# Optimization experiments

Measured on AMD Instinct MI355X. Metric: run time of the kernel, lower is better.

## Reference

```python
import jax, jax.numpy as jnp
import numpy as np

N = 16384      # number of PF candidates (nodes)
D_IN = 13      # pfc_input_dim
H = 16         # hidden_dim
K = 8          # kNN neighbors (includes self, dist 0, matching PyG knn(x, x, k))


def setup_inputs() -> dict:
    key = jax.random.key(0)
    ks = jax.random.split(key, 8)

    def w(k, shape):
        return (jax.random.normal(k, shape, dtype=jnp.float32) * 0.1)

    z = lambda n: jnp.zeros((n,), dtype=jnp.float32)
    return {
        "x_pfc": jax.random.normal(ks[0], (N, D_IN), dtype=jnp.float32),
        # pfc_encode: Linear(13,8) SiLU, Linear(8,16) SiLU, Linear(16,15)
        "W1": w(ks[1], (D_IN, H // 2)), "b1": z(H // 2),
        "W2": w(ks[2], (H // 2, H)),    "b2": z(H),
        "W3": w(ks[3], (H, H - 1)),     "b3": z(H - 1),
        # DynamicEdgeConv edge MLP: Linear(2H, H) SiLU
        "We": w(ks[4], (2 * H, H)),     "be": z(H),
        # ffn: Linear(H, 2H) SiLU, Linear(2H, H)
        "Wf1": w(ks[5], (H, 2 * H)),    "bf1": z(2 * H),
        "Wf2": w(ks[6], (2 * H, H)),    "bf2": z(H),
    }


def reference(x_pfc, W1, b1, W2, b2, W3, b3, We, be, Wf1, bf1, Wf2, bf2):
    silu = jax.nn.silu
    # pfc_encode (dropout = identity in eval)
    h = silu(x_pfc @ W1 + b1)
    h = silu(h @ W2 + b2)
    h = h @ W3 + b3                                   # [N, H-1]
    x = jnp.concatenate([h, x_pfc[:, -1:]], axis=1)   # [N, H]

    # Dynamic kNN graph in encoded-feature space (self included, dist 0)
    sq = jnp.sum(x * x, axis=1)                       # [N]
    d2 = sq[:, None] + sq[None, :] - 2.0 * (x @ x.T)  # [N, N] pairwise sq dist
    _, idx = jax.lax.top_k(-d2, K)                    # [N, K] neighbor indices

    # EdgeConv message: nn(cat([x_i, x_j - x_i])), mean aggregation
    x_j = x[idx]                                      # [N, K, H] gather
    x_i = x[:, None, :]                               # [N, 1, H]
    edge_in = jnp.concatenate(
        [jnp.broadcast_to(x_i, x_j.shape), x_j - x_i], axis=-1)  # [N, K, 2H]
    msg = silu(edge_in @ We + be)                     # [N, K, H]
    feats = jnp.mean(msg, axis=1)                     # [N, H]

    # ffn (dropout = identity in eval)
    f = silu(feats @ Wf1 + bf1)
    f = f @ Wf2 + bf2                                 # [N, H]
    return jnp.concatenate([f, x_pfc], axis=1)        # [N, H + D_IN]
```

## Files before the change

### kernel.cpp

```cpp
#include <hip/hip_runtime.h>
#include <math.h>

#define NPTS 16384
#define DIN 13
#define KNN 8
#define GL 12
#define BIGF 1.7014118e38f

typedef _Float16 half8 __attribute__((ext_vector_type(8)));
typedef float f32x4 __attribute__((ext_vector_type(4)));
typedef float f32x16 __attribute__((ext_vector_type(16)));

union HU4 { uint4 u; half8 h; };

__device__ __forceinline__ float silu(float v) {
    return v / (1.0f + __expf(-v));
}

#define MED3(v, a, b) __builtin_amdgcn_fmed3f((v), (a), (b))

#define INS8V(v) {                      \
    d7 = MED3((v), d6, d7);             \
    d6 = MED3((v), d5, d6);             \
    d5 = MED3((v), d4, d5);             \
    d4 = MED3((v), d3, d4);             \
    d3 = MED3((v), d2, d3);             \
    d2 = MED3((v), d1, d2);             \
    d1 = MED3((v), d0, d1);             \
    d0 = fminf((v), d0); }

#define INS12G(v) {                     \
    g11 = MED3((v), g10, g11);          \
    g10 = MED3((v), g9, g10);           \
    g9  = MED3((v), g8, g9);            \
    g8  = MED3((v), g7, g8);            \
    g7  = MED3((v), g6, g7);            \
    g6  = MED3((v), g5, g6);            \
    g5  = MED3((v), g4, g5);            \
    g4  = MED3((v), g3, g4);            \
    g3  = MED3((v), g2, g3);            \
    g2  = MED3((v), g1, g2);            \
    g1  = MED3((v), g0, g1);            \
    g0  = fminf((v), g0); }

#define CSW(p, q) { float lo_ = fminf(m##p, m##q); float hi_ = fmaxf(m##p, m##q); m##p = lo_; m##q = hi_; }

#define CLEAN16() \
    CSW(0,8) CSW(1,9) CSW(2,10) CSW(3,11) CSW(4,12) CSW(5,13) CSW(6,14) CSW(7,15) \
    CSW(0,4) CSW(1,5) CSW(2,6) CSW(3,7) CSW(8,12) CSW(9,13) CSW(10,14) CSW(11,15) \
    CSW(0,2) CSW(1,3) CSW(4,6) CSW(5,7) CSW(8,10) CSW(9,11) CSW(12,14) CSW(13,15) \
    CSW(0,1) CSW(2,3) CSW(4,5) CSW(6,7) CSW(8,9) CSW(10,11) CSW(12,13) CSW(14,15)

#define MERGE12_SHFL(mask) {                                  \
    float b0 = __shfl_xor(g0, (mask), 64);                    \
    float b1 = __shfl_xor(g1, (mask), 64);                    \
    float b2 = __shfl_xor(g2, (mask), 64);                    \
    float b3 = __shfl_xor(g3, (mask), 64);                    \
    float b4 = __shfl_xor(g4, (mask), 64);                    \
    float b5 = __shfl_xor(g5, (mask), 64);                    \
    float b6 = __shfl_xor(g6, (mask), 64);                    \
    float b7 = __shfl_xor(g7, (mask), 64);                    \
    float b8 = __shfl_xor(g8, (mask), 64);                    \
    float b9 = __shfl_xor(g9, (mask), 64);                    \
    float b10 = __shfl_xor(g10, (mask), 64);                  \
    float b11 = __shfl_xor(g11, (mask), 64);                  \
    float m0 = g0, m1 = g1, m2 = g2, m3 = g3;                 \
    float m4 = fminf(g4, b11), m5 = fminf(g5, b10);           \
    float m6 = fminf(g6, b9),  m7 = fminf(g7, b8);            \
    float m8 = fminf(g8, b7),  m9 = fminf(g9, b6);            \
    float m10 = fminf(g10, b5), m11 = fminf(g11, b4);         \
    float m12 = b3, m13 = b2, m14 = b1, m15 = b0;             \
    CLEAN16();                                                \
    g0 = m0; g1 = m1; g2 = m2; g3 = m3; g4 = m4; g5 = m5;     \
    g6 = m6; g7 = m7; g8 = m8; g9 = m9; g10 = m10; g11 = m11; }

#define MERGE12_LDS(LD) {                                     \
    float b0 = LD(0), b1 = LD(1), b2 = LD(2), b3 = LD(3);     \
    float b4 = LD(4), b5 = LD(5), b6 = LD(6), b7 = LD(7);     \
    float b8 = LD(8), b9 = LD(9), b10 = LD(10), b11 = LD(11); \
    float m0 = g0, m1 = g1, m2 = g2, m3 = g3;                 \
    float m4 = fminf(g4, b11), m5 = fminf(g5, b10);           \
    float m6 = fminf(g6, b9),  m7 = fminf(g7, b8);            \
    float m8 = fminf(g8, b7),  m9 = fminf(g9, b6);            \
    float m10 = fminf(g10, b5), m11 = fminf(g11, b4);         \
    float m12 = b3, m13 = b2, m14 = b1, m15 = b0;             \
    CLEAN16();                                                \
    g0 = m0; g1 = m1; g2 = m2; g3 = m3; g4 = m4; g5 = m5;     \
    g6 = m6; g7 = m7; g8 = m8; g9 = m9; g10 = m10; g11 = m11; }

#define MERGE8(mask) {                                   \
    float b0 = __shfl_xor(d0, (mask), 64);               \
    float b1 = __shfl_xor(d1, (mask), 64);               \
    float b2 = __shfl_xor(d2, (mask), 64);               \
    float b3 = __shfl_xor(d3, (mask), 64);               \
    float b4 = __shfl_xor(d4, (mask), 64);               \
    float b5 = __shfl_xor(d5, (mask), 64);               \
    float b6 = __shfl_xor(d6, (mask), 64);               \
    float b7 = __shfl_xor(d7, (mask), 64);               \
    float m0 = fminf(d0, b7), m1 = fminf(d1, b6);        \
    float m2 = fminf(d2, b5), m3 = fminf(d3, b4);        \
    float m4 = fminf(d4, b3), m5 = fminf(d5, b2);        \
    float m6 = fminf(d6, b1), m7 = fminf(d7, b0);        \
    CSW(0,4) CSW(1,5) CSW(2,6) CSW(3,7)                  \
    CSW(0,2) CSW(1,3) CSW(4,6) CSW(5,7)                  \
    CSW(0,1) CSW(2,3) CSW(4,5) CSW(6,7)                  \
    d0 = m0; d1 = m1; d2 = m2; d3 = m3;                  \
    d4 = m4; d5 = m5; d6 = m6; d7 = m7; }

__global__ __launch_bounds__(64) void k_encoder(
    const float* __restrict__ x_pfc,
    const float* __restrict__ W1, const float* __restrict__ b1,
    const float* __restrict__ W2, const float* __restrict__ b2,
    const float* __restrict__ W3, const float* __restrict__ b3,
    const float* __restrict__ We, const float* __restrict__ be,
    float* __restrict__ xo, _Float16* __restrict__ H, _Float16* __restrict__ L,
    _Float16* __restrict__ YH, _Float16* __restrict__ YL,
    float* __restrict__ SQF, unsigned* __restrict__ SQHL,
    float* __restrict__ ACC)
{
    __shared__ float sW1[DIN * 8];
    __shared__ float sb1[8];
    __shared__ float sW2[8 * 16];
    __shared__ float sb2[16];
    __shared__ float sW3[16 * 15];
    __shared__ float sb3[15];
    __shared__ float sWe[16 * 16];
    __shared__ float sbe[16];
    int t = threadIdx.x;
    for (int q = t; q < DIN * 8; q += 64) sW1[q] = W1[q];
    for (int q = t; q < 8; q += 64) sb1[q] = b1[q];
    for (int q = t; q < 8 * 16; q += 64) sW2[q] = W2[q];
    for (int q = t; q < 16; q += 64) sb2[q] = b2[q];
    for (int q = t; q < 16 * 15; q += 64) sW3[q] = W3[q];
    for (int q = t; q < 15; q += 64) sb3[q] = b3[q];
    for (int q = t; q < 16 * 16; q += 64) sWe[q] = We[q];
    for (int q = t; q < 16; q += 64) sbe[q] = be[q];
    __syncthreads();

    int i = blockIdx.x * 64 + t;
    float in[DIN];
#pragma unroll
    for (int d = 0; d < DIN; ++d) in[d] = x_pfc[i * DIN + d];

    float a1[8];
#pragma unroll
    for (int h = 0; h < 8; ++h) a1[h] = sb1[h];
#pragma unroll
    for (int d = 0; d < DIN; ++d) {
        float v = in[d];
#pragma unroll
        for (int h = 0; h < 8; ++h) a1[h] += v * sW1[d * 8 + h];
    }
#pragma unroll
    for (int h = 0; h < 8; ++h) a1[h] = silu(a1[h]);

    float a2[16];
#pragma unroll
    for (int h = 0; h < 16; ++h) a2[h] = sb2[h];
#pragma unroll
    for (int d = 0; d < 8; ++d) {
        float v = a1[d];
#pragma unroll
        for (int h = 0; h < 16; ++h) a2[h] += v * sW2[d * 16 + h];
    }
#pragma unroll
    for (int h = 0; h < 16; ++h) a2[h] = silu(a2[h]);

    float a3[15];
#pragma unroll
    for (int h = 0; h < 15; ++h) a3[h] = sb3[h];
#pragma unroll
    for (int d = 0; d < 16; ++d) {
        float v = a2[d];
#pragma unroll
        for (int h = 0; h < 15; ++h) a3[h] += v * sW3[d * 15 + h];
    }

    float xr[16];
#pragma unroll
    for (int h = 0; h < 15; ++h) xr[h] = a3[h];
    xr[15] = in[DIN - 1];

    float s = 0.0f;
#pragma unroll
    for (int d = 0; d < 16; ++d) s += xr[d] * xr[d];

    float accb[16];
#pragma unroll
    for (int h = 0; h < 16; ++h) accb[h] = sbe[h];
#pragma unroll
    for (int d = 0; d < 16; ++d) {
        float v = xr[d];
#pragma unroll
        for (int h = 0; h < 16; ++h) accb[h] += v * sWe[d * 16 + h];
    }

    _Float16 hb[16], lb[16], yhb[16], ylb[16];
#pragma unroll
    for (int d = 0; d < 16; ++d) {
        _Float16 h = (_Float16)xr[d];
        hb[d] = h;
        lb[d] = (_Float16)(xr[d] - (float)h);
        float y = -2.0f * xr[d];
        _Float16 yh = (_Float16)y;
        yhb[d] = yh;
        ylb[d] = (_Float16)(y - (float)yh);
    }
    {
        uint4* p;
        p = (uint4*)(H + (size_t)i * 16);  p[0] = ((uint4*)hb)[0];  p[1] = ((uint4*)hb)[1];
        p = (uint4*)(L + (size_t)i * 16);  p[0] = ((uint4*)lb)[0];  p[1] = ((uint4*)lb)[1];
        p = (uint4*)(YH + (size_t)i * 16); p[0] = ((uint4*)yhb)[0]; p[1] = ((uint4*)yhb)[1];
        p = (uint4*)(YL + (size_t)i * 16); p[0] = ((uint4*)ylb)[0]; p[1] = ((uint4*)ylb)[1];
        f32x4* xq = (f32x4*)(xo + (size_t)i * 16);
        f32x4* aq = (f32x4*)(ACC + (size_t)i * 16);
#pragma unroll
        for (int q = 0; q < 4; ++q) {
            f32x4 xv, av;
#pragma unroll
            for (int r = 0; r < 4; ++r) { xv[r] = xr[q * 4 + r]; av[r] = accb[q * 4 + r]; }
            xq[q] = xv;
            aq[q] = av;
        }
    }
    SQF[i] = s;
    {
        _Float16 sh = (_Float16)s;
        _Float16 sl = (_Float16)(s - (float)sh);
        unsigned uh = *(const unsigned short*)&sh;
        unsigned ul = *(const unsigned short*)&sl;
        SQHL[i] = (ul << 16) | uh;
    }
}

__global__ __launch_bounds__(512, 4) void k_knn(
    const _Float16* __restrict__ H, const _Float16* __restrict__ L,
    const _Float16* __restrict__ YH, const _Float16* __restrict__ YL,
    const float* __restrict__ SQF, unsigned* __restrict__ CV)
{
    __shared__ float sBuf[8192];

    int t = threadIdx.x;
    int w = t >> 6;
    int lane = t & 63;
    int r31 = lane & 31;
    int hh = lane >> 5;
    int ih = blockIdx.x >> 1;
    int jh = blockIdx.x & 1;
    int i0 = ih * 32;

    int gi = i0 + r31;
    half8 B1 = *(const half8*)(YH + (size_t)gi * 16 + hh * 8);
    half8 B2 = *(const half8*)(YL + (size_t)gi * 16 + hh * 8);

    {
        const f32x4* src = (const f32x4*)(SQF + jh * 8192);
        f32x4* dst = (f32x4*)sBuf;
        for (int q = t; q < 2048; q += 512) dst[q] = src[q];
    }

    float g0 = BIGF, g1 = BIGF, g2 = BIGF, g3 = BIGF;
    float g4 = BIGF, g5 = BIGF, g6 = BIGF, g7 = BIGF;
    float g8 = BIGF, g9 = BIGF, g10 = BIGF, g11 = BIGF;

    int jw = jh * 8192 + w * 1024;
    const _Float16* pH = H + ((size_t)(jw + r31)) * 16 + hh * 8;
    const _Float16* pL = L + ((size_t)(jw + r31)) * 16 + hh * 8;
    const float* sqb = sBuf + w * 1024 + hh * 4;
    unsigned idt = (unsigned)((w << 1) | hh);

    __syncthreads();

#pragma unroll 1
    for (int cc = 0; cc < 8; ++cc) {
        half8 Ah0 = *(const half8*)(pH);
        half8 Al0 = *(const half8*)(pL);
        half8 Ah1 = *(const half8*)(pH + 512);
        half8 Al1 = *(const half8*)(pL + 512);
        half8 Ah2 = *(const half8*)(pH + 1024);
        half8 Al2 = *(const half8*)(pL + 1024);
        half8 Ah3 = *(const half8*)(pH + 1536);
        half8 Al3 = *(const half8*)(pL + 1536);
        const float* sq4 = sqb + cc * 128;
        unsigned idc = idt + (unsigned)(cc << 6);

#define TILE(AH, AL, U) {                                                    \
        const f32x4* s_ = (const f32x4*)(sq4 + (U) * 32);                    \
        f32x4 s0 = s_[0], s1 = s_[2], s2 = s_[4], s3 = s_[6];                \
        f32x16 c;                                                            \
        c[0] = s0[0]; c[1] = s0[1]; c[2] = s0[2]; c[3] = s0[3];              \
        c[4] = s1[0]; c[5] = s1[1]; c[6] = s1[2]; c[7] = s1[3];              \
        c[8] = s2[0]; c[9] = s2[1]; c[10] = s2[2]; c[11] = s2[3];            \
        c[12] = s3[0]; c[13] = s3[1]; c[14] = s3[2]; c[15] = s3[3];          \
        c = __builtin_amdgcn_mfma_f32_32x32x16_f16(AH, B1, c, 0, 0, 0);      \
        c = __builtin_amdgcn_mfma_f32_32x32x16_f16(AL, B1, c, 0, 0, 0);      \
        c = __builtin_amdgcn_mfma_f32_32x32x16_f16(AH, B2, c, 0, 0, 0);      \
        float v0 = fminf(fminf(c[0], c[1]), c[2]);                           \
        float v1 = fminf(fminf(c[3], c[4]), c[5]);                           \
        float v2 = fminf(fminf(c[6], c[7]), c[8]);                           \
        float v3 = fminf(fminf(c[9], c[10]), c[11]);                         \
        float v4 = fminf(fminf(c[12], c[13]), c[14]);                        \
        float v5 = fminf(fminf(v0, v1), c[15]);                              \
        float v6 = fminf(fminf(v2, v3), v4);                                 \
        float vmin = fminf(v5, v6);                                          \
        unsigned pk = (__float_as_uint(vmin) & 0xFFFFFC00u)                  \
                    | (idc + (unsigned)((U) << 4));                          \
        float pf = __uint_as_float(pk);                                      \
        INS12G(pf); }

        TILE(Ah0, Al0, 0)
        TILE(Ah1, Al1, 1)
        TILE(Ah2, Al2, 2)
        TILE(Ah3, Al3, 3)
#undef TILE
        pH += 2048;
        pL += 2048;
    }

    MERGE12_SHFL(32);

    __syncthreads();

#define STORE12() if (lane < 32) {                       \
        sBuf[(w * GL + 0) * 32 + r31] = g0;              \
        sBuf[(w * GL + 1) * 32 + r31] = g1;              \
        sBuf[(w * GL + 2) * 32 + r31] = g2;              \
        sBuf[(w * GL + 3) * 32 + r31] = g3;              \
        sBuf[(w * GL + 4) * 32 + r31] = g4;              \
        sBuf[(w * GL + 5) * 32 + r31] = g5;              \
        sBuf[(w * GL + 6) * 32 + r31] = g6;              \
        sBuf[(w * GL + 7) * 32 + r31] = g7;              \
        sBuf[(w * GL + 8) * 32 + r31] = g8;              \
        sBuf[(w * GL + 9) * 32 + r31] = g9;              \
        sBuf[(w * GL + 10) * 32 + r31] = g10;            \
        sBuf[(w * GL + 11) * 32 + r31] = g11; }

    if (w >= 4) STORE12();
    __syncthreads();
    if (w < 4) {
        int pw = w + 4;
#define LD(s) sBuf[(pw * GL + (s)) * 32 + r31]
        MERGE12_LDS(LD);
#undef LD
    }
    __syncthreads();
    if (w == 2 || w == 3) STORE12();
    __syncthreads();
    if (w < 2) {
        int pw = w + 2;
#define LD(s) sBuf[(pw * GL + (s)) * 32 + r31]
        MERGE12_LDS(LD);
#undef LD
    }
    __syncthreads();
    if (w == 1) STORE12();
    __syncthreads();
    if (w == 0) {
        int pw = 1;
#define LD(s) sBuf[(pw * GL + (s)) * 32 + r31]
        MERGE12_LDS(LD);
#undef LD
        if (lane < 32) {
            unsigned jb = ((unsigned)jh) << 9;
            size_t base = ((size_t)jh * NPTS + (i0 + r31)) * GL;
            CV[base + 0] = __float_as_uint(g0) | jb;
            CV[base + 1] = __float_as_uint(g1) | jb;
            CV[base + 2] = __float_as_uint(g2) | jb;
            CV[base + 3] = __float_as_uint(g3) | jb;
            CV[base + 4] = __float_as_uint(g4) | jb;
            CV[base + 5] = __float_as_uint(g5) | jb;
            CV[base + 6] = __float_as_uint(g6) | jb;
            CV[base + 7] = __float_as_uint(g7) | jb;
            CV[base + 8] = __float_as_uint(g8) | jb;
            CV[base + 9] = __float_as_uint(g9) | jb;
            CV[base + 10] = __float_as_uint(g10) | jb;
            CV[base + 11] = __float_as_uint(g11) | jb;
        }
    }
#undef STORE12
}

__global__ __launch_bounds__(512, 4) void k_head(
    const float* __restrict__ x, const unsigned* __restrict__ CV,
    const float* __restrict__ SQF,
    const float* __restrict__ x_pfc, const float* __restrict__ ACC,
    const float* __restrict__ We,
    const float* __restrict__ Wf1, const float* __restrict__ bf1,
    const float* __restrict__ Wf2, const float* __restrict__ bf2,
    float* __restrict__ out)
{
    __shared__ float sWe2[16 * 16];
    __shared__ float sWf1[16 * 32];
    __shared__ float sbf1[32];
    __shared__ float sWf2[32 * 16];
    __shared__ float sbf2[16];
    __shared__ int sGrp[32][GL];
    __shared__ int cnt[32];
    __shared__ int sIdx[32 * 8];
    __shared__ float sF1[32 * 33];
    int t = threadIdx.x;
    for (int q = t; q < 16 * 16; q += 512) sWe2[q] = We[256 + q];
    for (int q = t; q < 16 * 32; q += 512) sWf1[q] = Wf1[q];
    for (int q = t; q < 32; q += 512) sbf1[q] = bf1[q];
    for (int q = t; q < 32 * 16; q += 512) sWf2[q] = Wf2[q];
    for (int q = t; q < 16; q += 512) sbf2[q] = bf2[q];

    int i0 = blockIdx.x * 32;

    if (t < 64) {
        int pi = t & 31;
        int hf = t >> 5;
        const f32x4* c = (const f32x4*)(CV + ((size_t)hf * NPTS + (i0 + pi)) * GL);
        f32x4 c0 = c[0], c1 = c[1], c2 = c[2];
        float g0 = c0[0], g1 = c0[1], g2 = c0[2], g3 = c0[3];
        float g4 = c1[0], g5 = c1[1], g6 = c1[2], g7 = c1[3];
        float g8 = c2[0], g9 = c2[1], g10 = c2[2], g11 = c2[3];
        MERGE12_SHFL(32);
        if (t < 32) {
            cnt[pi] = 0;
#define DECJB(gk, s) { unsigned id_ = __float_as_uint(gk) & 0x3FFu;          \
            sGrp[pi][s] = (int)(((id_ >> 9) & 1) * 8192 + ((id_ >> 1) & 7) * 1024 + \
                                ((id_ >> 4) & 31) * 32 + (id_ & 1) * 4); }
            DECJB(g0, 0) DECJB(g1, 1) DECJB(g2, 2) DECJB(g3, 3)
            DECJB(g4, 4) DECJB(g5, 5) DECJB(g6, 6) DECJB(g7, 7)
            DECJB(g8, 8) DECJB(g9, 9) DECJB(g10, 10) DECJB(g11, 11)
#undef DECJB
        }
    }
    __syncthreads();

    int l = t & 15;
    int pt = t >> 4;
    int ql = l & 3;
    int qd = l >> 2;
    int i = i0 + pt;

    float xi[16];
    {
        const f32x4* xiv = (const f32x4*)(x + (size_t)i * 16);
#pragma unroll
        for (int q = 0; q < 4; ++q) {
            f32x4 a = xiv[q];
#pragma unroll
            for (int r = 0; r < 4; ++r) xi[q * 4 + r] = a[r];
        }
    }
    f32x4 xiq = ((const f32x4*)(x + (size_t)i * 16))[ql];

    float val[12];
    float d0 = BIGF, d1 = BIGF, d2 = BIGF, d3 = BIGF;
    float d4 = BIGF, d5 = BIGF, d6 = BIGF, d7 = BIGF;
#pragma unroll
    for (int g = 0; g < GL; ++g) {
        int jb = sGrp[pt][g];
        float vg = BIGF;
#pragma unroll
        for (int rho = 0; rho < 4; ++rho) {
            f32x4 a = *((const f32x4*)(x + ((size_t)(jb + rho * 8)) * 16) + l);
            float qdot = xiq[0] * a[0];
            qdot = fmaf(xiq[1], a[1], qdot);
            qdot = fmaf(xiq[2], a[2], qdot);
            qdot = fmaf(xiq[3], a[3], qdot);
            qdot += __shfl_xor(qdot, 1, 64);
            qdot += __shfl_xor(qdot, 2, 64);
            float v = fmaf(qdot, -2.0f, SQF[jb + rho * 8 + qd]);
            vg = (ql == rho) ? v : vg;
        }
        val[g] = vg;
        INS8V(vg);
    }

    MERGE8(1);
    MERGE8(2);
    MERGE8(4);
    MERGE8(8);
    float kth = d7;

#pragma unroll
    for (int g = 0; g < GL; ++g) {
        float v = val[g];
        if (v <= kth) {
            int j = sGrp[pt][g] + ql * 8 + qd;
            int p = atomicAdd(&cnt[pt], 1);
            if (p < KNN) sIdx[pt * 8 + p] = j;
        }
    }
    __syncthreads();

    int e8 = l & 7;
    int j = sIdx[pt * 8 + e8];

    float xd[16];
    {
        const f32x4* xjv = (const f32x4*)(x + (size_t)j * 16);
#pragma unroll
        for (int q = 0; q < 4; ++q) {
            f32x4 a = xjv[q];
#pragma unroll
            for (int r = 0; r < 4; ++r) xd[q * 4 + r] = a[r] - xi[q * 4 + r];
        }
    }

    float acc[16];
    {
        const f32x4* av = (const f32x4*)(ACC + (size_t)i * 16);
#pragma unroll
        for (int q = 0; q < 4; ++q) {
            f32x4 a = av[q];
#pragma unroll
            for (int r = 0; r < 4; ++r) acc[q * 4 + r] = a[r];
        }
    }
#pragma unroll
    for (int d = 0; d < 16; ++d) {
        float v = xd[d];
#pragma unroll
        for (int h = 0; h < 16; ++h) acc[h] += v * sWe2[d * 16 + h];
    }

    float feats[16];
#pragma unroll
    for (int h = 0; h < 16; ++h) feats[h] = silu(acc[h]);

#pragma unroll
    for (int mask = 1; mask <= 4; mask <<= 1) {
#pragma unroll
        for (int h = 0; h < 16; ++h) feats[h] += __shfl_xor(feats[h], mask, 64);
    }
#pragma unroll
    for (int h = 0; h < 16; ++h) feats[h] *= 0.125f;

    float p0 = sbf1[l];
    float p1 = sbf1[l + 16];
#pragma unroll
    for (int k = 0; k < 16; ++k) {
        float v = feats[k];
        p0 = fmaf(v, sWf1[k * 32 + l], p0);
        p1 = fmaf(v, sWf1[k * 32 + l + 16], p1);
    }
    p0 = silu(p0);
    p1 = silu(p1);
    sF1[pt * 33 + l] = p0;
    sF1[pt * 33 + 16 + l] = p1;
    __syncthreads();

    float o = sbf2[l];
#pragma unroll
    for (int k = 0; k < 32; ++k)
        o = fmaf(sF1[pt * 33 + k], sWf2[k * 16 + l], o);

    out[(size_t)i * 29 + l] = o;
    if (l < DIN) out[(size_t)i * 29 + 16 + l] = x_pfc[i * DIN + l];
}

extern "C" void kernel_launch(void* const* d_in, const int* in_sizes, int n_in,
                              void* d_out, int out_size, void* d_ws, size_t ws_size,
                              hipStream_t stream)
{
    const float* x_pfc = (const float*)d_in[0];
    const float* W1 = (const float*)d_in[1];
    const float* b1 = (const float*)d_in[2];
    const float* W2 = (const float*)d_in[3];
    const float* b2 = (const float*)d_in[4];
    const float* W3 = (const float*)d_in[5];
    const float* b3 = (const float*)d_in[6];
    const float* We = (const float*)d_in[7];
    const float* be = (const float*)d_in[8];
    const float* Wf1 = (const float*)d_in[9];
    const float* bf1 = (const float*)d_in[10];
    const float* Wf2 = (const float*)d_in[11];
    const float* bf2 = (const float*)d_in[12];
    float* out = (float*)d_out;

    float* xw = (float*)d_ws;
    float* ACCa = xw + (size_t)NPTS * 16;
    _Float16* Ha = (_Float16*)(ACCa + (size_t)NPTS * 16);
    _Float16* La = Ha + (size_t)NPTS * 16;
    _Float16* YHa = La + (size_t)NPTS * 16;
    _Float16* YLa = YHa + (size_t)NPTS * 16;
    float* SQFa = (float*)(YLa + (size_t)NPTS * 16);
    unsigned* SQHLa = (unsigned*)(SQFa + NPTS);
    unsigned* CVa = SQHLa + NPTS;

    hipLaunchKernelGGL(k_encoder, dim3(NPTS / 64), dim3(64), 0, stream,
                       x_pfc, W1, b1, W2, b2, W3, b3, We, be,
                       xw, Ha, La, YHa, YLa, SQFa, SQHLa, ACCa);
    hipLaunchKernelGGL(k_knn, dim3(NPTS / 32 * 2), dim3(512), 0, stream,
                       Ha, La, YHa, YLa, SQFa, CVa);
    hipLaunchKernelGGL(k_head, dim3(NPTS / 32), dim3(512), 0, stream,
                       xw, CVa, SQFa, x_pfc, ACCa, We, Wf1, bf1, Wf2, bf2, out);
}
```

Measured before the change: 152.9 us.

## Software-pipeline kNN tile loads and raise occupancy hint to 6 blocks

Restructures the kNN distance loop so the next two tiles' A-fragments are loaded from global memory while the current two tiles run through MFMA and top-k insertion. The loop now handles two tiles per iteration instead of four loaded at once, with a peeled final iteration. The launch bound's min-blocks value goes from 4 to 6, which pushes the compiler toward fewer registers per thread. The tighter register budget could cause spills or limit how far the loads get ahead of their use.

```diff
diff --git a/kernel.cpp b/kernel.cpp
--- a/kernel.cpp
+++ b/kernel.cpp
@@ -12,6 +12,7 @@
 typedef float f32x16 __attribute__((ext_vector_type(16)));
 
 union HU4 { uint4 u; half8 h; };
+union C16 { f32x16 w; f32x4 q[4]; };
 
 __device__ __forceinline__ float silu(float v) {
     return v / (1.0f + __expf(-v));
@@ -233,7 +234,7 @@
     }
 }
 
-__global__ __launch_bounds__(512, 4) void k_knn(
+__global__ __launch_bounds__(512, 6) void k_knn(
     const _Float16* __restrict__ H, const _Float16* __restrict__ L,
     const _Float16* __restrict__ YH, const _Float16* __restrict__ YL,
     const float* __restrict__ SQF, unsigned* __restrict__ CV)
@@ -271,51 +272,54 @@
 
     __syncthreads();
 
-#pragma unroll 1
-    for (int cc = 0; cc < 8; ++cc) {
-        half8 Ah0 = *(const half8*)(pH);
-        half8 Al0 = *(const half8*)(pL);
-        half8 Ah1 = *(const half8*)(pH + 512);
-        half8 Al1 = *(const half8*)(pL + 512);
-        half8 Ah2 = *(const half8*)(pH + 1024);
-        half8 Al2 = *(const half8*)(pL + 1024);
-        half8 Ah3 = *(const half8*)(pH + 1536);
-        half8 Al3 = *(const half8*)(pL + 1536);
-        const float* sq4 = sqb + cc * 128;
-        unsigned idc = idt + (unsigned)(cc << 6);
-
-#define TILE(AH, AL, U) {                                                    \
-        const f32x4* s_ = (const f32x4*)(sq4 + (U) * 32);                    \
-        f32x4 s0 = s_[0], s1 = s_[2], s2 = s_[4], s3 = s_[6];                \
-        f32x16 c;                                                            \
-        c[0] = s0[0]; c[1] = s0[1]; c[2] = s0[2]; c[3] = s0[3];              \
-        c[4] = s1[0]; c[5] = s1[1]; c[6] = s1[2]; c[7] = s1[3];              \
-        c[8] = s2[0]; c[9] = s2[1]; c[10] = s2[2]; c[11] = s2[3];            \
-        c[12] = s3[0]; c[13] = s3[1]; c[14] = s3[2]; c[15] = s3[3];          \
-        c = __builtin_amdgcn_mfma_f32_32x32x16_f16(AH, B1, c, 0, 0, 0);      \
-        c = __builtin_amdgcn_mfma_f32_32x32x16_f16(AL, B1, c, 0, 0, 0);      \
-        c = __builtin_amdgcn_mfma_f32_32x32x16_f16(AH, B2, c, 0, 0, 0);      \
-        float v0 = fminf(fminf(c[0], c[1]), c[2]);                           \
-        float v1 = fminf(fminf(c[3], c[4]), c[5]);                           \
-        float v2 = fminf(fminf(c[6], c[7]), c[8]);                           \
-        float v3 = fminf(fminf(c[9], c[10]), c[11]);                         \
-        float v4 = fminf(fminf(c[12], c[13]), c[14]);                        \
-        float v5 = fminf(fminf(v0, v1), c[15]);                              \
+#define TILE(AH, AL, SQ4, IDC, U) {                                          \
+        const f32x4* s_ = (const f32x4*)((SQ4) + (U) * 32);                  \
+        C16 c;                                                               \
+        c.q[0] = s_[0]; c.q[1] = s_[2]; c.q[2] = s_[4]; c.q[3] = s_[6];      \
+        c.w = __builtin_amdgcn_mfma_f32_32x32x16_f16(AH, B1, c.w, 0, 0, 0);  \
+        c.w = __builtin_amdgcn_mfma_f32_32x32x16_f16(AL, B1, c.w, 0, 0, 0);  \
+        c.w = __builtin_amdgcn_mfma_f32_32x32x16_f16(AH, B2, c.w, 0, 0, 0);  \
+        float v0 = fminf(fminf(c.w[0], c.w[1]), c.w[2]);                     \
+        float v1 = fminf(fminf(c.w[3], c.w[4]), c.w[5]);                     \
+        float v2 = fminf(fminf(c.w[6], c.w[7]), c.w[8]);                     \
+        float v3 = fminf(fminf(c.w[9], c.w[10]), c.w[11]);                   \
+        float v4 = fminf(fminf(c.w[12], c.w[13]), c.w[14]);                  \
+        float v5 = fminf(fminf(v0, v1), c.w[15]);                            \
         float v6 = fminf(fminf(v2, v3), v4);                                 \
         float vmin = fminf(v5, v6);                                          \
         unsigned pk = (__float_as_uint(vmin) & 0xFFFFFC00u)                  \
-                    | (idc + (unsigned)((U) << 4));                          \
+                    | ((IDC) + (unsigned)((U) << 4));                        \
         float pf = __uint_as_float(pk);                                      \
         INS12G(pf); }
 
-        TILE(Ah0, Al0, 0)
-        TILE(Ah1, Al1, 1)
-        TILE(Ah2, Al2, 2)
-        TILE(Ah3, Al3, 3)
+    half8 cAh0 = *(const half8*)(pH);
+    half8 cAl0 = *(const half8*)(pL);
+    half8 cAh1 = *(const half8*)(pH + 512);
+    half8 cAl1 = *(const half8*)(pL + 512);
+
+#pragma unroll 1
+    for (int cc = 0; cc < 15; ++cc) {
+        half8 nAh0 = *(const half8*)(pH + 1024);
+        half8 nAl0 = *(const half8*)(pL + 1024);
+        half8 nAh1 = *(const half8*)(pH + 1536);
+        half8 nAl1 = *(const half8*)(pL + 1536);
+
+        const float* sq4 = sqb + cc * 64;
+        unsigned idc = idt + (unsigned)(cc << 5);
+        TILE(cAh0, cAl0, sq4, idc, 0)
+        TILE(cAh1, cAl1, sq4, idc, 1)
+
+        cAh0 = nAh0; cAl0 = nAl0; cAh1 = nAh1; cAl1 = nAl1;
+        pH += 1024;
+        pL += 1024;
+    }
+    {
+        const float* sq4 = sqb + 15 * 64;
+        unsigned idc = idt + (unsigned)(15 << 5);
+        TILE(cAh0, cAl0, sq4, idc, 0)
+        TILE(cAh1, cAl1, sq4, idc, 1)
+    }
 #undef TILE
-        pH += 2048;
-        pL += 2048;
-    }
 
     MERGE12_SHFL(32);
 
```

Measured after the change: 152.1 us. About the same (-0.5%).
